# Optimization experiments

Measured on AMD Instinct MI355X. Metric: run time of the kernel, lower is better.

## Reference

```python
import jax, jax.numpy as jnp
import numpy as np

B, D_MODEL, HIDEEN, HEAD, IMG_H, IMG_W = 16, 512, 512, 8, 32, 32
D_K = D_MODEL // HEAD
EPS = 1e-5


def setup_inputs() -> dict:
    key = jax.random.key(0)
    ks = jax.random.split(key, 9)
    s_in = 1.0 / np.sqrt(D_MODEL)
    s_h = 1.0 / np.sqrt(HIDEEN)
    return {
        "x": jax.random.normal(ks[0], (B, D_MODEL, IMG_H, IMG_W), jnp.float32),
        "Wq": jax.random.uniform(ks[1], (HIDEEN, D_MODEL), jnp.float32, -s_in, s_in),
        "bq": jax.random.uniform(ks[2], (HIDEEN,), jnp.float32, -s_in, s_in),
        "Wk": jax.random.uniform(ks[3], (HIDEEN, D_MODEL), jnp.float32, -s_in, s_in),
        "bk": jax.random.uniform(ks[4], (HIDEEN,), jnp.float32, -s_in, s_in),
        "Wv": jax.random.uniform(ks[5], (HIDEEN, D_MODEL), jnp.float32, -s_in, s_in),
        "bv": jax.random.uniform(ks[6], (HIDEEN,), jnp.float32, -s_in, s_in),
        "Wo": jax.random.uniform(ks[7], (HIDEEN, HIDEEN), jnp.float32, -s_h, s_h),
        "bo": jax.random.uniform(ks[8], (HIDEEN,), jnp.float32, -s_h, s_h),
    }


def _conv1x1(x, W, b):
    # x: [B, Cin, H, W], W: [Cout, Cin]
    return jnp.einsum("bchw,oc->bohw", x, W) + b[None, :, None, None]


def _heads(t):
    # torch: [B, C, H, W] -> view(B, -1, head, d_k) -> transpose(1, 2)
    return t.reshape(B, -1, HEAD, D_K).transpose(0, 2, 1, 3)  # [B, head, N, d_k]


def reference(x, Wq, bq, Wk, bk, Wv, bv, Wo, bo):
    q = _heads(_conv1x1(x, Wq, bq))
    k = _heads(_conv1x1(x, Wk, bk))
    v = _heads(_conv1x1(x, Wv, bv))
    scores = jnp.einsum("bhnd,bhmd->bhnm", q, k) / np.sqrt(D_K).astype(np.float32)
    attn = jax.nn.softmax(scores, axis=-1)
    out = jnp.einsum("bhnm,bhmd->bhnd", attn, v)  # [B, head, N, d_k]
    # back to image layout: [B, N, head*d_k] -> [B, hideen, H, W]
    out = out.transpose(0, 2, 1, 3).reshape(B, -1, HEAD * D_K)
    out = out.transpose(0, 2, 1).reshape(B, -1, IMG_H, IMG_W)
    out = _conv1x1(out, Wo, bo)
    # InstanceNorm2d (affine=False, biased var, eps=1e-5)
    mu = out.mean(axis=(2, 3), keepdims=True)
    var = out.var(axis=(2, 3), keepdims=True)
    out = (out - mu) / jnp.sqrt(var + EPS)
    # original applies the SAME attn_out conv a second time
    out = _conv1x1(out, Wo, bo)
    return out
```

## Files before the change

kernel.cpp:

```cpp
#include <hip/hip_runtime.h>


typedef short bf16x8_t __attribute__((ext_vector_type(8)));
typedef float f32x4_t  __attribute__((ext_vector_type(4)));

union U4 {
  uint4 u;
  bf16x8_t v;
  unsigned short us[8];
};

__device__ __forceinline__ unsigned short f2bf(float f) {
  union { float f; unsigned int u; } x; x.f = f;
  unsigned int r = x.u + 0x7fffu + ((x.u >> 16) & 1u);
  return (unsigned short)(r >> 16);
}

#define AS1 __attribute__((address_space(1)))
#define AS3 __attribute__((address_space(3)))

__device__ __forceinline__ void gload16(const unsigned short* g,
                                        unsigned short* l) {
  __builtin_amdgcn_global_load_lds((const AS1 unsigned int*)g,
                                   (AS3 unsigned int*)l, 16, 0, 0);
}

#define BATCH_STRIDE (512 * 1024)

__global__ __launch_bounds__(256) void cvtx_k(
    const float* __restrict__ x, unsigned short* __restrict__ xb)
{
  __shared__ float tile[32][33];
  const int b = blockIdx.z, c0 = blockIdx.y * 32, n0 = blockIdx.x * 32;
  const int t = threadIdx.x;
  {
    const int cl_ = t >> 3, n4 = (t & 7) * 4;
    const float4 u = *(const float4*)(x + (size_t)b * BATCH_STRIDE
                                      + (size_t)(c0 + cl_) * 1024 + n0 + n4);
    tile[cl_][n4] = u.x; tile[cl_][n4 + 1] = u.y;
    tile[cl_][n4 + 2] = u.z; tile[cl_][n4 + 3] = u.w;
  }
  __syncthreads();
  {
    const int nl = t >> 3, c4 = (t & 7) * 4;
    ushort4 o;
    o.x = f2bf(tile[c4][nl]);     o.y = f2bf(tile[c4 + 1][nl]);
    o.z = f2bf(tile[c4 + 2][nl]); o.w = f2bf(tile[c4 + 3][nl]);
    *(ushort4*)(xb + (size_t)b * BATCH_STRIDE + (size_t)(n0 + nl) * 512
                + c0 + c4) = o;
  }
}

__global__ __launch_bounds__(256) void cvtw_k(
    const float* __restrict__ s0, const float* __restrict__ s1,
    const float* __restrict__ s2, unsigned short* __restrict__ dst)
{
  const float* s = (blockIdx.y == 0) ? s0 : (blockIdx.y == 1) ? s1 : s2;
  const int i = (blockIdx.x * 256 + threadIdx.x) * 8;
  const float4 a = *(const float4*)(s + i);
  const float4 c = *(const float4*)(s + i + 4);
  U4 o;
  o.us[0] = f2bf(a.x); o.us[1] = f2bf(a.y);
  o.us[2] = f2bf(a.z); o.us[3] = f2bf(a.w);
  o.us[4] = f2bf(c.x); o.us[5] = f2bf(c.y);
  o.us[6] = f2bf(c.z); o.us[7] = f2bf(c.w);
  *(uint4*)(dst + (size_t)blockIdx.y * 262144 + i) = o.u;
}

template<int OUTF>
__device__ __forceinline__ void gemm_core(
    const unsigned short* __restrict__ Wb, const float* __restrict__ bias,
    const unsigned short* __restrict__ src, void* __restrict__ dst,
    int m0, int n0, int b, float scale,
    unsigned short* sA, unsigned short* sB)
{
  const int t = threadIdx.x;
  const int lane = t & 63, wv = t >> 6, qd = lane >> 4, cl = lane & 15;
  const int wm = wv >> 1, wn = wv & 1;
  const unsigned short* srcb = src + (size_t)b * BATCH_STRIDE + (size_t)n0 * 512;
  const unsigned short* wrow = Wb + (size_t)m0 * 512;

  const int lr = lane >> 2, ls = (lane & 3) * 8;
  const int r0 = wv * 32;

  f32x4_t acc[4][4];
  #pragma unroll
  for (int i = 0; i < 4; ++i)
    #pragma unroll
    for (int f = 0; f < 4; ++f) acc[i][f] = (f32x4_t){0.f, 0.f, 0.f, 0.f};

  for (int kk = 0; kk < 512; kk += 32) {
    if (kk) __syncthreads();
    gload16(wrow + (size_t)(r0 + lr) * 512 + kk + ls,      sA + r0 * 32);
    gload16(wrow + (size_t)(r0 + 16 + lr) * 512 + kk + ls, sA + (r0 + 16) * 32);
    gload16(srcb + (size_t)(r0 + lr) * 512 + kk + ls,      sB + r0 * 32);
    gload16(srcb + (size_t)(r0 + 16 + lr) * 512 + kk + ls, sB + (r0 + 16) * 32);
    __syncthreads();

    U4 af[4], bf[4];
    #pragma unroll
    for (int i = 0; i < 4; ++i) {
      af[i].u = *(const uint4*)(sA + (wm * 64 + i * 16 + cl) * 32 + qd * 8);
      bf[i].u = *(const uint4*)(sB + (wn * 64 + i * 16 + cl) * 32 + qd * 8);
    }
    #pragma unroll
    for (int i = 0; i < 4; ++i)
      #pragma unroll
      for (int f = 0; f < 4; ++f)
        acc[i][f] = __builtin_amdgcn_mfma_f32_16x16x32_bf16(
            af[i].v, bf[f].v, acc[i][f], 0, 0, 0);
  }

  #pragma unroll
  for (int i = 0; i < 4; ++i) {
    #pragma unroll
    for (int r = 0; r < 4; ++r) {
      const int o = m0 + wm * 64 + i * 16 + qd * 4 + r;
      const float bv = bias[o];
      #pragma unroll
      for (int f = 0; f < 4; ++f) {
        const int n = n0 + wn * 64 + f * 16 + cl;
        const size_t idx = (size_t)b * BATCH_STRIDE + (size_t)o * 1024 + n;
        const float val = (acc[i][f][r] + bv) * scale;
        if (OUTF) ((float*)dst)[idx] = val;
        else      ((unsigned short*)dst)[idx] = f2bf(val);
      }
    }
  }
}

struct QKVArgs {
  const unsigned short* W[3];
  const float* bias[3];
  unsigned short* dst[3];
  float scale[3];
};

__global__ __launch_bounds__(256) void qkv_k(
    QKVArgs args, const unsigned short* __restrict__ xb)
{
  __shared__ __align__(16) unsigned short sA[128 * 32];
  __shared__ __align__(16) unsigned short sB[128 * 32];
  const int widx = blockIdx.y >> 2;
  const int m0 = (blockIdx.y & 3) * 128;
  gemm_core<0>(args.W[widx], args.bias[widx], xb, args.dst[widx],
               m0, blockIdx.x * 128, blockIdx.z, args.scale[widx], sA, sB);
}

template<int OUTF>
__global__ __launch_bounds__(256) void gemm_wo_k(
    const unsigned short* __restrict__ Wb, const float* __restrict__ bias,
    const unsigned short* __restrict__ src, void* __restrict__ dst)
{
  __shared__ __align__(16) unsigned short sA[128 * 32];
  __shared__ __align__(16) unsigned short sB[128 * 32];
  gemm_core<OUTF>(Wb, bias, src, dst, blockIdx.y * 128, blockIdx.x * 128,
                  blockIdx.z, 1.0f, sA, sB);
}

__global__ __launch_bounds__(256) void vt_k(
    const unsigned short* __restrict__ src, unsigned short* __restrict__ dst)
{
  __shared__ unsigned short tile[32][36];
  const int b = blockIdx.z, j0 = blockIdx.y * 32, p0 = blockIdx.x * 32;
  const int t = threadIdx.x;
  {
    const int pr = t >> 3, jc = (t & 7) * 4;
    *(ushort4*)&tile[pr][jc] = *(const ushort4*)(
        src + (size_t)b * BATCH_STRIDE + (size_t)(p0 + pr) * 512 + j0 + jc);
  }
  __syncthreads();
  {
    const int jr = t >> 3, pc = (t & 7) * 4;
    ushort4 o;
    o.x = tile[pc][jr];     o.y = tile[pc + 1][jr];
    o.z = tile[pc + 2][jr]; o.w = tile[pc + 3][jr];
    *(ushort4*)(dst + (size_t)b * BATCH_STRIDE + (size_t)(j0 + jr) * 1024
                + p0 + pc) = o;
  }
}

__global__ __launch_bounds__(256) void attn_k(
    const unsigned short* __restrict__ Q,
    const unsigned short* __restrict__ K,
    const unsigned short* __restrict__ Vt,
    unsigned short* __restrict__ O)
{
  __shared__ __align__(16) unsigned short sK2[2][64 * 64];
  __shared__ __align__(16) unsigned short sV2[2][64 * 64];
  __shared__ __align__(16) unsigned short sP[4 * 16 * 72];

  const int t = threadIdx.x;
  const int lane = t & 63, wv = t >> 6, qd = lane >> 4, cl = lane & 15;

  const int g = blockIdx.y * 16 + blockIdx.x;
  const int xcd = g & 7, rest = g >> 3;
  const int iblk = rest & 15;
  const int bh = (rest >> 4) * 8 + xcd;
  const int b = bh >> 3, h = bh & 7;
  const int i0 = iblk * 64;
  const size_t bbase = (size_t)b * BATCH_STRIDE;
  const int hoff = h * 64;

  U4 aq0, aq1;
  {
    const unsigned short* qp =
        Q + bbase + (size_t)(i0 + wv * 16 + cl) * 512 + hoff + qd * 8;
    aq0.u = *(const uint4*)qp;
    aq1.u = *(const uint4*)(qp + 32);
  }

  const int lrow = lane >> 3;
  const int lchk = ((lane & 7) ^ lrow) * 8;
  const int sw = cl & 7;
  const int c0r = (qd ^ sw) * 8;
  const int c1r = ((qd + 4) ^ sw) * 8;

  f32x4_t oacc[4];
  #pragma unroll
  for (int f = 0; f < 4; ++f) oacc[f] = (f32x4_t){0.f, 0.f, 0.f, 0.f};
  float rs[4] = {0.f, 0.f, 0.f, 0.f};

  #pragma unroll
  for (int p = 0; p < 2; ++p) {
    const int r = wv * 16 + p * 8;
    gload16(K + bbase + (size_t)(r + lrow) * 512 + hoff + lchk,
            &sK2[0][r * 64]);
    gload16(Vt + bbase + (size_t)(hoff + r + lrow) * 1024 + lchk,
            &sV2[0][r * 64]);
  }
  __syncthreads();

  for (int tt = 0; tt < 16; ++tt) {
    const unsigned short* sKb = sK2[tt & 1];
    const unsigned short* sVb = sV2[tt & 1];

    if (tt < 15) {
      const int jn = (tt + 1) * 64;
      unsigned short* dK = sK2[(tt + 1) & 1];
      unsigned short* dV = sV2[(tt + 1) & 1];
      #pragma unroll
      for (int p = 0; p < 2; ++p) {
        const int r = wv * 16 + p * 8;
        gload16(K + bbase + (size_t)(jn + r + lrow) * 512 + hoff + lchk,
                dK + r * 64);
        gload16(Vt + bbase + (size_t)(hoff + r + lrow) * 1024 + jn + lchk,
                dV + r * 64);
      }
    }

    f32x4_t s[4];
    __builtin_amdgcn_s_setprio(1);
    #pragma unroll
    for (int nh = 0; nh < 4; ++nh) {
      s[nh] = (f32x4_t){0.f, 0.f, 0.f, 0.f};
      U4 bk0; bk0.u = *(const uint4*)(sKb + (nh * 16 + cl) * 64 + c0r);
      U4 bk1; bk1.u = *(const uint4*)(sKb + (nh * 16 + cl) * 64 + c1r);
      s[nh] = __builtin_amdgcn_mfma_f32_16x16x32_bf16(aq0.v, bk0.v, s[nh], 0, 0, 0);
      s[nh] = __builtin_amdgcn_mfma_f32_16x16x32_bf16(aq1.v, bk1.v, s[nh], 0, 0, 0);
    }
    __builtin_amdgcn_s_setprio(0);

    #pragma unroll
    for (int nh = 0; nh < 4; ++nh) {
      #pragma unroll
      for (int r = 0; r < 4; ++r) {
        const float pv = __expf(s[nh][r]);
        sP[wv * 1152 + (qd * 4 + r) * 72 + nh * 16 + cl] = f2bf(pv);
        rs[r] += pv;
      }
    }

    asm volatile("s_waitcnt lgkmcnt(0)" ::: "memory");
    __builtin_amdgcn_sched_barrier(0);

    U4 pf0, pf1;
    pf0.u = *(const uint4*)(sP + wv * 1152 + cl * 72 + qd * 8);
    pf1.u = *(const uint4*)(sP + wv * 1152 + cl * 72 + 32 + qd * 8);
    __builtin_amdgcn_s_setprio(1);
    #pragma unroll
    for (int f = 0; f < 4; ++f) {
      U4 vf0, vf1;
      vf0.u = *(const uint4*)(sVb + (f * 16 + cl) * 64 + c0r);
      vf1.u = *(const uint4*)(sVb + (f * 16 + cl) * 64 + c1r);
      oacc[f] = __builtin_amdgcn_mfma_f32_16x16x32_bf16(pf0.v, vf0.v, oacc[f], 0, 0, 0);
      oacc[f] = __builtin_amdgcn_mfma_f32_16x16x32_bf16(pf1.v, vf1.v, oacc[f], 0, 0, 0);
    }
    __builtin_amdgcn_s_setprio(0);

    __syncthreads();
  }

  #pragma unroll
  for (int m = 1; m < 16; m <<= 1)
    #pragma unroll
    for (int r = 0; r < 4; ++r) rs[r] += __shfl_xor(rs[r], m);

  #pragma unroll
  for (int f = 0; f < 4; ++f) {
    #pragma unroll
    for (int r = 0; r < 4; ++r) {
      const int i = i0 + wv * 16 + qd * 4 + r;
      const int j = hoff + f * 16 + cl;
      O[bbase + (size_t)i * 512 + j] = f2bf(oacc[f][r] / rs[r]);
    }
  }
}

__global__ __launch_bounds__(256) void norm_k(
    const float* __restrict__ x, unsigned short* __restrict__ y)
{
  __shared__ float tile[8][1028];
  __shared__ float shm[8], shv[8];
  const int b = blockIdx.x >> 6, c0 = (blockIdx.x & 63) * 8;
  const int t = threadIdx.x;
  const int ch = t >> 5, ln = t & 31;
  const float* xr = x + (size_t)b * BATCH_STRIDE + (size_t)(c0 + ch) * 1024;
  float s1 = 0.f, s2 = 0.f;
  #pragma unroll
  for (int j = 0; j < 8; ++j) {
    const int n = ln * 4 + j * 128;
    const float4 u = *(const float4*)(xr + n);
    tile[ch][n] = u.x; tile[ch][n + 1] = u.y;
    tile[ch][n + 2] = u.z; tile[ch][n + 3] = u.w;
    s1 += u.x + u.y + u.z + u.w;
    s2 += u.x * u.x + u.y * u.y + u.z * u.z + u.w * u.w;
  }
  #pragma unroll
  for (int m = 1; m < 32; m <<= 1) {
    s1 += __shfl_xor(s1, m);
    s2 += __shfl_xor(s2, m);
  }
  if (ln == 0) {
    const float mean = s1 * (1.f / 1024.f);
    const float var = s2 * (1.f / 1024.f) - mean * mean;
    shm[ch] = mean;
    shv[ch] = rsqrtf(var + 1e-5f);
  }
  __syncthreads();
  unsigned short* yb = y + (size_t)b * BATCH_STRIDE;
  #pragma unroll
  for (int jn = 0; jn < 4; ++jn) {
    const int n = t + jn * 256;
    U4 o;
    #pragma unroll
    for (int c = 0; c < 8; ++c)
      o.us[c] = f2bf((tile[c][n] - shm[c]) * shv[c]);
    *(uint4*)(yb + (size_t)n * 512 + c0) = o.u;
  }
}

extern "C" void kernel_launch(void* const* d_in, const int* in_sizes, int n_in,
                              void* d_out, int out_size, void* d_ws, size_t ws_size,
                              hipStream_t stream) {
  const float* x  = (const float*)d_in[0];
  const float* Wq = (const float*)d_in[1];
  const float* bq = (const float*)d_in[2];
  const float* Wk = (const float*)d_in[3];
  const float* bk = (const float*)d_in[4];
  const float* Wv = (const float*)d_in[5];
  const float* bv = (const float*)d_in[6];
  const float* Wo = (const float*)d_in[7];
  const float* bo = (const float*)d_in[8];

  const size_t BUF = (size_t)16 * BATCH_STRIDE;
  unsigned short* xb = (unsigned short*)d_ws;
  unsigned short* Qb = xb + BUF;
  unsigned short* Kb = Qb + BUF;
  unsigned short* Vb = (unsigned short*)d_out;
  unsigned short* Ob = Vb + BUF;
  unsigned short* Vt = xb;
  float*          out1f = (float*)d_ws;
  unsigned short* out1n = Kb;

  unsigned short* Wbf3 = Ob;
  unsigned short* WoA  = Vb;
  unsigned short* WoB  = xb;

  QKVArgs qa;
  qa.W[0] = Wbf3; qa.W[1] = Wbf3 + 262144; qa.W[2] = Wbf3 + 524288;
  qa.bias[0] = bq; qa.bias[1] = bk; qa.bias[2] = bv;
  qa.dst[0] = Qb; qa.dst[1] = Kb; qa.dst[2] = Vb;
  qa.scale[0] = 0.125f; qa.scale[1] = 1.0f; qa.scale[2] = 1.0f;

  cvtx_k<<<dim3(32, 16, 16), 256, 0, stream>>>(x, xb);
  cvtw_k<<<dim3(128, 3), 256, 0, stream>>>(Wq, Wk, Wv, Wbf3);
  qkv_k<<<dim3(8, 12, 16), 256, 0, stream>>>(qa, xb);
  vt_k<<<dim3(32, 16, 16), 256, 0, stream>>>(Vb, Vt);
  cvtw_k<<<dim3(128, 1), 256, 0, stream>>>(Wo, Wo, Wo, WoA);
  attn_k<<<dim3(16, 128), 256, 0, stream>>>(Qb, Kb, Vt, Ob);
  gemm_wo_k<1><<<dim3(8, 4, 16), 256, 0, stream>>>(WoA, bo, Ob, out1f);
  norm_k<<<dim3(16 * 64), 256, 0, stream>>>(out1f, out1n);
  cvtw_k<<<dim3(128, 1), 256, 0, stream>>>(Wo, Wo, Wo, WoB);
  gemm_wo_k<1><<<dim3(8, 4, 16), 256, 0, stream>>>(WoB, bo, out1n, d_out);
}
```

Before: 264.7 us.

## Replace K/V double-buffering with single buffers and split refill points

```diff
diff --git a/kernel.cpp b/kernel.cpp
--- a/kernel.cpp
+++ b/kernel.cpp
@@ -186,8 +186,8 @@
     const unsigned short* __restrict__ Vt,
     unsigned short* __restrict__ O)
 {
-  __shared__ __align__(16) unsigned short sK2[2][64 * 64];
-  __shared__ __align__(16) unsigned short sV2[2][64 * 64];
+  __shared__ __align__(16) unsigned short sK[64 * 64];
+  __shared__ __align__(16) unsigned short sV[64 * 64];
   __shared__ __align__(16) unsigned short sP[4 * 16 * 72];
 
   const int t = threadIdx.x;
@@ -224,42 +224,34 @@
   #pragma unroll
   for (int p = 0; p < 2; ++p) {
     const int r = wv * 16 + p * 8;
-    gload16(K + bbase + (size_t)(r + lrow) * 512 + hoff + lchk,
-            &sK2[0][r * 64]);
-    gload16(Vt + bbase + (size_t)(hoff + r + lrow) * 1024 + lchk,
-            &sV2[0][r * 64]);
+    gload16(K + bbase + (size_t)(r + lrow) * 512 + hoff + lchk, sK + r * 64);
+    gload16(Vt + bbase + (size_t)(hoff + r + lrow) * 1024 + lchk, sV + r * 64);
   }
   __syncthreads();
 
   for (int tt = 0; tt < 16; ++tt) {
-    const unsigned short* sKb = sK2[tt & 1];
-    const unsigned short* sVb = sV2[tt & 1];
-
+    f32x4_t s[4];
+    __builtin_amdgcn_s_setprio(1);
+    #pragma unroll
+    for (int nh = 0; nh < 4; ++nh) {
+      s[nh] = (f32x4_t){0.f, 0.f, 0.f, 0.f};
+      U4 bk0; bk0.u = *(const uint4*)(sK + (nh * 16 + cl) * 64 + c0r);
+      U4 bk1; bk1.u = *(const uint4*)(sK + (nh * 16 + cl) * 64 + c1r);
+      s[nh] = __builtin_amdgcn_mfma_f32_16x16x32_bf16(aq0.v, bk0.v, s[nh], 0, 0, 0);
+      s[nh] = __builtin_amdgcn_mfma_f32_16x16x32_bf16(aq1.v, bk1.v, s[nh], 0, 0, 0);
+    }
+    __builtin_amdgcn_s_setprio(0);
+
+    __syncthreads();
     if (tt < 15) {
       const int jn = (tt + 1) * 64;
-      unsigned short* dK = sK2[(tt + 1) & 1];
-      unsigned short* dV = sV2[(tt + 1) & 1];
       #pragma unroll
       for (int p = 0; p < 2; ++p) {
         const int r = wv * 16 + p * 8;
         gload16(K + bbase + (size_t)(jn + r + lrow) * 512 + hoff + lchk,
-                dK + r * 64);
-        gload16(Vt + bbase + (size_t)(hoff + r + lrow) * 1024 + jn + lchk,
-                dV + r * 64);
+                sK + r * 64);
       }
     }
-
-    f32x4_t s[4];
-    __builtin_amdgcn_s_setprio(1);
-    #pragma unroll
-    for (int nh = 0; nh < 4; ++nh) {
-      s[nh] = (f32x4_t){0.f, 0.f, 0.f, 0.f};
-      U4 bk0; bk0.u = *(const uint4*)(sKb + (nh * 16 + cl) * 64 + c0r);
-      U4 bk1; bk1.u = *(const uint4*)(sKb + (nh * 16 + cl) * 64 + c1r);
-      s[nh] = __builtin_amdgcn_mfma_f32_16x16x32_bf16(aq0.v, bk0.v, s[nh], 0, 0, 0);
-      s[nh] = __builtin_amdgcn_mfma_f32_16x16x32_bf16(aq1.v, bk1.v, s[nh], 0, 0, 0);
-    }
-    __builtin_amdgcn_s_setprio(0);
 
     #pragma unroll
     for (int nh = 0; nh < 4; ++nh) {
@@ -281,14 +273,23 @@
     #pragma unroll
     for (int f = 0; f < 4; ++f) {
       U4 vf0, vf1;
-      vf0.u = *(const uint4*)(sVb + (f * 16 + cl) * 64 + c0r);
-      vf1.u = *(const uint4*)(sVb + (f * 16 + cl) * 64 + c1r);
+      vf0.u = *(const uint4*)(sV + (f * 16 + cl) * 64 + c0r);
+      vf1.u = *(const uint4*)(sV + (f * 16 + cl) * 64 + c1r);
       oacc[f] = __builtin_amdgcn_mfma_f32_16x16x32_bf16(pf0.v, vf0.v, oacc[f], 0, 0, 0);
       oacc[f] = __builtin_amdgcn_mfma_f32_16x16x32_bf16(pf1.v, vf1.v, oacc[f], 0, 0, 0);
     }
     __builtin_amdgcn_s_setprio(0);
 
     __syncthreads();
+    if (tt < 15) {
+      const int jn = (tt + 1) * 64;
+      #pragma unroll
+      for (int p = 0; p < 2; ++p) {
+        const int r = wv * 16 + p * 8;
+        gload16(Vt + bbase + (size_t)(hoff + r + lrow) * 1024 + jn + lchk,
+                sV + r * 64);
+      }
+    }
   }
 
   #pragma unroll
```

Result: faster. 257.6 us (-2.7%).
